# Kernel optimization log

Hardware: AMD Instinct MI355X
Metric: run time of the kernel (lower is better)

## Reference

```python
import jax, jax.numpy as jnp
import numpy as np

N_NODES = 50000
N_EDGES = 800000
N_GRAPHS = 128


def _gcn_conv(x, W, b, src, dst, n_nodes):
    # PyG GCNConv: h = x @ W; add self-loops; symmetric norm; aggregate; + bias
    h = x @ W  # [N, out]
    loop = jnp.arange(n_nodes, dtype=src.dtype)
    src_all = jnp.concatenate([src, loop])  # source (row)
    dst_all = jnp.concatenate([dst, loop])  # target (col)
    ones = jnp.ones(src_all.shape[0], dtype=h.dtype)
    deg = jax.ops.segment_sum(ones, dst_all, num_segments=n_nodes)  # in-degree w/ self loops
    dis = jnp.where(deg > 0, jax.lax.rsqrt(deg), 0.0)
    norm = dis[src_all] * dis[dst_all]  # [E+N]
    msg = norm[:, None] * h[src_all]  # [E+N, out]
    out = jax.ops.segment_sum(msg, dst_all, num_segments=n_nodes)
    return out + b


def setup_inputs() -> dict:
    key = jax.random.key(0)
    ks = jax.random.split(key, 7)
    x = jax.random.normal(ks[0], (N_NODES, 4), dtype=jnp.float32)
    edge_index = jax.random.randint(ks[1], (2, N_EDGES), 0, N_NODES, dtype=jnp.int64)
    batch = jnp.sort(jax.random.randint(ks[2], (N_NODES,), 0, N_GRAPHS, dtype=jnp.int64))
    # Glorot-ish init for the linear weights, zeros for bias (PyG default)
    W1 = jax.random.normal(ks[3], (4, 64), dtype=jnp.float32) * (1.0 / np.sqrt(4))
    b1 = jnp.zeros((64,), dtype=jnp.float32)
    W2 = jax.random.normal(ks[4], (64, 64), dtype=jnp.float32) * (1.0 / np.sqrt(64))
    b2 = jnp.zeros((64,), dtype=jnp.float32)
    return {"x": x, "edge_index": edge_index, "batch": batch, "num_graphs": N_GRAPHS,
            "W1": W1, "b1": b1, "W2": W2, "b2": b2}


def reference(x, edge_index, batch, num_graphs, W1, b1, W2, b2):
    src, dst = edge_index[0], edge_index[1]
    n = x.shape[0]
    h = jax.nn.relu(_gcn_conv(x, W1, b1, src, dst, n))
    h = jax.nn.relu(_gcn_conv(h, W2, b2, src, dst, n))
    # global_mean_pool: segment mean over graph ids
    sums = jax.ops.segment_sum(h, batch, num_segments=num_graphs)  # [G, 64]
    cnts = jax.ops.segment_sum(jnp.ones((n,), dtype=h.dtype), batch, num_segments=num_graphs)
    return sums / jnp.maximum(cnts, 1.0)[:, None]
```

## Files before the change

### kernel.cpp

```cpp
#include <hip/hip_runtime.h>
#include <hip/hip_fp16.h>

#define NG 128
#define CHUNK 4096

__device__ __forceinline__ int wave_iscan(int v, int lane) {
#pragma unroll
  for (int off = 1; off < 64; off <<= 1) {
    int u = __shfl_up(v, off, 64);
    if (lane >= off) v += u;
  }
  return v;
}


__global__ void bsum_kernel(const int* __restrict__ src, int* __restrict__ bsum, int M) {
  __shared__ int wsum[4];
  int tid = threadIdx.x, lane = tid & 63, wid = tid >> 6;
  int i = blockIdx.x * 256 + tid;
  int v = (i < M) ? src[i] : 0;
  int inc = wave_iscan(v, lane);
  if (lane == 63) wsum[wid] = inc;
  __syncthreads();
  if (tid == 0) bsum[blockIdx.x] = wsum[0] + wsum[1] + wsum[2] + wsum[3];
}

__global__ void bscan_kernel(int* __restrict__ bsum, int nb) {
  __shared__ int wsum[16];
  int tid = threadIdx.x, lane = tid & 63, wid = tid >> 6;
  int v = (tid < nb) ? bsum[tid] : 0;
  int inc = wave_iscan(v, lane);
  if (lane == 63) wsum[wid] = inc;
  __syncthreads();
  if (tid == 0) {
    int a = 0;
#pragma unroll
    for (int w = 0; w < 16; ++w) { int t = wsum[w]; wsum[w] = a; a += t; }
  }
  __syncthreads();
  if (tid < nb) bsum[tid] = inc - v + wsum[wid];
}

__global__ void offadd_kernel(int* __restrict__ off, const int* __restrict__ bsum, int M) {
  __shared__ int wsum[4];
  int tid = threadIdx.x, lane = tid & 63, wid = tid >> 6;
  int i = blockIdx.x * 256 + tid;
  int v = (i < M) ? off[i] : 0;
  int inc = wave_iscan(v, lane);
  if (lane == 63) wsum[wid] = inc;
  __syncthreads();
  if (tid == 0) {
    int a = bsum[blockIdx.x];
#pragma unroll
    for (int w = 0; w < 4; ++w) { int t = wsum[w]; wsum[w] = a; a += t; }
  }
  __syncthreads();
  if (i < M) off[i] = inc - v + wsum[wid];
}


__global__ void hist_kernel(const int* __restrict__ ei, int E, int nblkE, int K,
                            int* __restrict__ off) {
  __shared__ int lh[256];
  int tid = threadIdx.x, blk = blockIdx.x;
  lh[tid] = 0;
  __syncthreads();
  int e0 = blk * CHUNK;
  const int4* d4 = (const int4*)(ei + E + e0);
  for (int i = tid; i < CHUNK / 4; i += 256) {
    int base = e0 + 4 * i;
    if (base + 3 < E) {
      int4 d = d4[i];
      atomicAdd(&lh[d.x >> 8], 1);
      atomicAdd(&lh[d.y >> 8], 1);
      atomicAdd(&lh[d.z >> 8], 1);
      atomicAdd(&lh[d.w >> 8], 1);
    } else {
#pragma unroll
      for (int j = 0; j < 4; ++j) {
        int e = base + j;
        if (e < E) atomicAdd(&lh[ei[E + e] >> 8], 1);
      }
    }
  }
  __syncthreads();
  if (tid < K) off[tid * nblkE + blk] = lh[tid];
}

__global__ void part_kernel(const int* __restrict__ ei, int E, int nblkE, int K,
                            const int* __restrict__ off, unsigned int* __restrict__ epack) {
  __shared__ int lcur[256];
  int tid = threadIdx.x, blk = blockIdx.x;
  if (tid < K) lcur[tid] = off[tid * nblkE + blk];
  __syncthreads();
  int e0 = blk * CHUNK;
  const int4* s4 = (const int4*)(ei + e0);
  const int4* d4 = (const int4*)(ei + E + e0);
  for (int i = tid; i < CHUNK / 4; i += 256) {
    int base = e0 + 4 * i;
    if (base + 3 < E) {
      int4 s = s4[i];
      int4 d = d4[i];
#pragma unroll
      for (int j = 0; j < 4; ++j) {
        unsigned int ss = (unsigned int)((j == 0) ? s.x : (j == 1) ? s.y : (j == 2) ? s.z : s.w);
        unsigned int dd = (unsigned int)((j == 0) ? d.x : (j == 1) ? d.y : (j == 2) ? d.z : d.w);
        int pos = atomicAdd(&lcur[dd >> 8], 1);
        epack[pos] = (ss << 8) | (dd & 255u);
      }
    } else {
#pragma unroll
      for (int j = 0; j < 4; ++j) {
        int e = base + j;
        if (e < E) {
          unsigned int ss = (unsigned int)ei[e], dd = (unsigned int)ei[E + e];
          int pos = atomicAdd(&lcur[dd >> 8], 1);
          epack[pos] = (ss << 8) | (dd & 255u);
        }
      }
    }
  }
}

__global__ void csr2_kernel(const int* __restrict__ off, int nblkE, int K,
                            const unsigned int* __restrict__ epack,
                            const float* __restrict__ x, int* __restrict__ deg,
                            int* __restrict__ rowptr, float* __restrict__ dis,
                            float* __restrict__ xs, unsigned short* __restrict__ esrc,
                            int N, int E) {
  __shared__ int lcnt[256];
  __shared__ int lcur[256];
  __shared__ int wsum[4];
  int tid = threadIdx.x, b = blockIdx.x;
  int lane = tid & 63, wid = tid >> 6;
  lcnt[tid] = 0;
  __syncthreads();
  int be0 = off[b * nblkE];
  int be1 = (b + 1 < K) ? off[(b + 1) * nblkE] : E;
  for (int i = be0 + tid; i < be1; i += 256) atomicAdd(&lcnt[epack[i] & 255u], 1);
  __syncthreads();
  int v = lcnt[tid];
  int inc = wave_iscan(v, lane);
  if (lane == 63) wsum[wid] = inc;
  __syncthreads();
  if (tid == 0) {
    int a = be0;
#pragma unroll
    for (int w = 0; w < 4; ++w) { int t = wsum[w]; wsum[w] = a; a += t; }
  }
  __syncthreads();
  int exc = inc - v + wsum[wid];
  lcur[tid] = exc;
  int node = (b << 8) + tid;
  if (node < N) {
    rowptr[node] = exc;
    deg[node] = v;
    float di = rsqrtf((float)v + 1.0f);
    dis[node] = di;
    float4 xv = ((const float4*)x)[node];
    ((float4*)xs)[node] = make_float4(di * xv.x, di * xv.y, di * xv.z, di * xv.w);
  }
  __syncthreads();
  for (int i = be0 + tid; i < be1; i += 256) {
    unsigned int pk = epack[i];
    int pos = atomicAdd(&lcur[pk & 255u], 1);
    esrc[pos] = (unsigned short)(pk >> 8);
  }
}

__global__ void __launch_bounds__(256, 8)
l1_kernel(const int* __restrict__ rowptr, const int* __restrict__ deg,
          const unsigned short* __restrict__ esrc, const float* __restrict__ xs,
          const float* __restrict__ x, const float* __restrict__ dis,
          const float* __restrict__ W1, const float* __restrict__ b1,
          __half* __restrict__ h1p, int N) {
  int tid = threadIdx.x;
  int lane = tid & 63, wid = tid >> 6;
  int d = __builtin_amdgcn_readfirstlane(blockIdx.x * 4 + wid);
  if (d >= N) return;
  float di = dis[d];
  int p = __builtin_amdgcn_readfirstlane(rowptr[d]);
  int n = __builtin_amdgcn_readfirstlane(deg[d]);
  float a0 = 0.f, a1 = 0.f, a2 = 0.f, a3 = 0.f;
  for (int k = lane; k < n; k += 64) {
    int e = esrc[p + k];
    float4 v = ((const float4*)xs)[e];
    a0 += v.x; a1 += v.y; a2 += v.z; a3 += v.w;
  }
  if (lane == 0) {
    float4 xv = ((const float4*)x)[d];
    a0 = fmaf(di, xv.x, a0); a1 = fmaf(di, xv.y, a1);
    a2 = fmaf(di, xv.z, a2); a3 = fmaf(di, xv.w, a3);
  }
#pragma unroll
  for (int off = 1; off < 64; off <<= 1) {
    a0 += __shfl_xor(a0, off, 64);
    a1 += __shfl_xor(a1, off, 64);
    a2 += __shfl_xor(a2, off, 64);
    a3 += __shfl_xor(a3, off, 64);
  }
  a0 *= di; a1 *= di; a2 *= di; a3 *= di;
  float o = b1[lane] + a0 * W1[lane] + a1 * W1[64 + lane] + a2 * W1[128 + lane] + a3 * W1[192 + lane];
  h1p[(size_t)d * 64 + lane] = __float2half(di * fmaxf(o, 0.0f));
}

__global__ void __launch_bounds__(256, 8)
l2_kernel(const int* __restrict__ rowptr, const int* __restrict__ deg,
          const unsigned short* __restrict__ esrc, const __half* __restrict__ h1p,
          const float* __restrict__ dis, const float* __restrict__ W2,
          const float* __restrict__ b2, const int* __restrict__ batch,
          float* __restrict__ gsum, int N) {
  __shared__ __align__(16) unsigned short ebuf[4][64];
  __shared__ float vbuf[4][64];
  __shared__ float obuf[4][64];
  __shared__ int gbuf[4];
  int tid = threadIdx.x;
  int lane = tid & 63, wid = tid >> 6;
  int g = lane >> 3, c = lane & 7;
  int d0 = blockIdx.x * 4 + wid;
  bool valid = d0 < N;
  int d = __builtin_amdgcn_readfirstlane(valid ? d0 : N - 1);
  float di = dis[d];
  int p = __builtin_amdgcn_readfirstlane(rowptr[d]);
  int n = __builtin_amdgcn_readfirstlane(deg[d]);
  float a0, a1, a2, a3, a4, a5, a6, a7;
  {
    float ms = (g == 0) ? 1.0f : 0.0f;
    uint4 w = *(const uint4*)(h1p + (size_t)d * 64 + 8 * c);
    float2 f0 = __half22float2(*(__half2*)&w.x);
    float2 f1 = __half22float2(*(__half2*)&w.y);
    float2 f2 = __half22float2(*(__half2*)&w.z);
    float2 f3 = __half22float2(*(__half2*)&w.w);
    a0 = ms * f0.x; a1 = ms * f0.y; a2 = ms * f1.x; a3 = ms * f1.y;
    a4 = ms * f2.x; a5 = ms * f2.y; a6 = ms * f3.x; a7 = ms * f3.y;
  }
  for (int base = 0; base < n; base += 64) {
    int m64 = n - base;
    if (m64 > 64) m64 = 64;
    ebuf[wid][lane] = esrc[p + base + ((lane < m64) ? lane : (m64 - 1))];
    for (int k = 0; k < m64; k += 8) {
      int e = ebuf[wid][k + g];
      float m = (k + g < m64) ? 1.0f : 0.0f;
      uint4 w = *(const uint4*)(h1p + (size_t)e * 64 + 8 * c);
      float2 f0 = __half22float2(*(__half2*)&w.x);
      float2 f1 = __half22float2(*(__half2*)&w.y);
      float2 f2 = __half22float2(*(__half2*)&w.z);
      float2 f3 = __half22float2(*(__half2*)&w.w);
      a0 = fmaf(m, f0.x, a0); a1 = fmaf(m, f0.y, a1);
      a2 = fmaf(m, f1.x, a2); a3 = fmaf(m, f1.y, a3);
      a4 = fmaf(m, f2.x, a4); a5 = fmaf(m, f2.y, a5);
      a6 = fmaf(m, f3.x, a6); a7 = fmaf(m, f3.y, a7);
    }
  }
#pragma unroll
  for (int off = 8; off < 64; off <<= 1) {
    a0 += __shfl_xor(a0, off, 64); a1 += __shfl_xor(a1, off, 64);
    a2 += __shfl_xor(a2, off, 64); a3 += __shfl_xor(a3, off, 64);
    a4 += __shfl_xor(a4, off, 64); a5 += __shfl_xor(a5, off, 64);
    a6 += __shfl_xor(a6, off, 64); a7 += __shfl_xor(a7, off, 64);
  }
  if (g == 0) {
    *(float4*)&vbuf[wid][8 * c] = make_float4(di * a0, di * a1, di * a2, di * a3);
    *(float4*)&vbuf[wid][8 * c + 4] = make_float4(di * a4, di * a5, di * a6, di * a7);
  }
  float o = b2[lane];
  const float4* vb4 = (const float4*)vbuf[wid];
#pragma unroll
  for (int kk = 0; kk < 16; ++kk) {
    float4 vv = vb4[kk];
    o = fmaf(vv.x, W2[(kk * 4 + 0) * 64 + lane], o);
    o = fmaf(vv.y, W2[(kk * 4 + 1) * 64 + lane], o);
    o = fmaf(vv.z, W2[(kk * 4 + 2) * 64 + lane], o);
    o = fmaf(vv.w, W2[(kk * 4 + 3) * 64 + lane], o);
  }
  obuf[wid][lane] = fmaxf(o, 0.0f);
  if (lane == 0) gbuf[wid] = valid ? batch[d] : -1;
  __syncthreads();
  if (wid == 0) {
    float s = 0.0f;
    int cur = gbuf[0];
#pragma unroll
    for (int r = 0; r < 4; ++r) {
      int gg = gbuf[r];
      if (gg != cur) {
        if (cur >= 0) atomicAdd(&gsum[cur * 64 + lane], s);
        s = 0.0f;
        cur = gg;
      }
      if (gg >= 0) s += obuf[r][lane];
    }
    if (cur >= 0) atomicAdd(&gsum[cur * 64 + lane], s);
  }
}


__device__ __forceinline__ int lbound(const int* __restrict__ a, int n, int v) {
  int lo = 0, hi = n;
  while (lo < hi) {
    int mid = (lo + hi) >> 1;
    if (a[mid] < v) lo = mid + 1; else hi = mid;
  }
  return lo;
}

__global__ void out_kernel(const float* __restrict__ gsum, const int* __restrict__ batch,
                           int N, float* __restrict__ out) {
  int t = blockIdx.x * blockDim.x + threadIdx.x;
  if (t >= NG * 64) return;
  int g = t >> 6;
  int cnt = lbound(batch, N, g + 1) - lbound(batch, N, g);
  out[t] = gsum[t] / fmaxf((float)cnt, 1.0f);
}


extern "C" void kernel_launch(void* const* d_in, const int* in_sizes, int n_in,
                              void* d_out, int out_size, void* d_ws, size_t ws_size,
                              hipStream_t stream) {
  const float* x = (const float*)d_in[0];
  const int* ei = (const int*)d_in[1];
  const int* batch = (const int*)d_in[2];
  const float* W1 = (const float*)d_in[4];
  const float* b1 = (const float*)d_in[5];
  const float* W2 = (const float*)d_in[6];
  const float* b2 = (const float*)d_in[7];

  const int N = in_sizes[0] / 4;
  const int E = in_sizes[1] / 2;
  const int K = (N + 255) >> 8;
  const int nblkE = (E + CHUNK - 1) / CHUNK;
  const int M2 = K * nblkE;
  const int NB2 = (M2 + 255) / 256;

  float* gsum = (float*)d_ws;
  int* deg = (int*)(gsum + 64 * NG);
  int* rowptr = deg + N;
  float* xs = (float*)(rowptr + N);
  float* dis = xs + (size_t)4 * N;
  __half* h1p = (__half*)(dis + N);
  unsigned short* esrc = (unsigned short*)(dis + N + (size_t)32 * N);
  int* off = (int*)(esrc + E);
  int* bsum2 = off + M2;
  unsigned int* epack = (unsigned int*)(bsum2 + 1024);

  hipMemsetAsync(d_ws, 0, (size_t)64 * NG * 4, stream);

  const int B = 256;
  hist_kernel<<<nblkE, 256, 0, stream>>>(ei, E, nblkE, K, off);
  bsum_kernel<<<NB2, 256, 0, stream>>>(off, bsum2, M2);
  bscan_kernel<<<1, 1024, 0, stream>>>(bsum2, NB2);
  offadd_kernel<<<NB2, 256, 0, stream>>>(off, bsum2, M2);
  part_kernel<<<nblkE, 256, 0, stream>>>(ei, E, nblkE, K, off, epack);
  csr2_kernel<<<K, 256, 0, stream>>>(off, nblkE, K, epack, x, deg, rowptr, dis, xs, esrc, N, E);
  l1_kernel<<<(N + 3) / 4, 256, 0, stream>>>(rowptr, deg, esrc, xs, x, dis, W1, b1, h1p, N);
  l2_kernel<<<(N + 3) / 4, 256, 0, stream>>>(rowptr, deg, esrc, h1p, dis, W2, b2, batch, gsum, N);
  out_kernel<<<(NG * 64 + B - 1) / B, B, 0, stream>>>(gsum, batch, N, (float*)d_out);
}
```

Baseline: 104.4 us.

## Replace three-kernel offset scan with global bucket counts and atomic cursors

The per-chunk-per-bucket offset matrix and its three-kernel multi-block scan are replaced by global bucket counts accumulated with atomics, a single small scan kernel, and a partition kernel that recomputes its local histogram and reserves ranges through atomics on global bucket cursors. This removes two kernel launches and the large offset array traffic. In exchange the partition kernel reads destination indices twice, and edge order within a bucket now depends on atomic ordering, so the result is no longer deterministic.

```diff
diff --git a/kernel.cpp b/kernel.cpp
--- a/kernel.cpp
+++ b/kernel.cpp
@@ -13,54 +13,8 @@
   return v;
 }
 
-
-__global__ void bsum_kernel(const int* __restrict__ src, int* __restrict__ bsum, int M) {
-  __shared__ int wsum[4];
-  int tid = threadIdx.x, lane = tid & 63, wid = tid >> 6;
-  int i = blockIdx.x * 256 + tid;
-  int v = (i < M) ? src[i] : 0;
-  int inc = wave_iscan(v, lane);
-  if (lane == 63) wsum[wid] = inc;
-  __syncthreads();
-  if (tid == 0) bsum[blockIdx.x] = wsum[0] + wsum[1] + wsum[2] + wsum[3];
-}
-
-__global__ void bscan_kernel(int* __restrict__ bsum, int nb) {
-  __shared__ int wsum[16];
-  int tid = threadIdx.x, lane = tid & 63, wid = tid >> 6;
-  int v = (tid < nb) ? bsum[tid] : 0;
-  int inc = wave_iscan(v, lane);
-  if (lane == 63) wsum[wid] = inc;
-  __syncthreads();
-  if (tid == 0) {
-    int a = 0;
-#pragma unroll
-    for (int w = 0; w < 16; ++w) { int t = wsum[w]; wsum[w] = a; a += t; }
-  }
-  __syncthreads();
-  if (tid < nb) bsum[tid] = inc - v + wsum[wid];
-}
-
-__global__ void offadd_kernel(int* __restrict__ off, const int* __restrict__ bsum, int M) {
-  __shared__ int wsum[4];
-  int tid = threadIdx.x, lane = tid & 63, wid = tid >> 6;
-  int i = blockIdx.x * 256 + tid;
-  int v = (i < M) ? off[i] : 0;
-  int inc = wave_iscan(v, lane);
-  if (lane == 63) wsum[wid] = inc;
-  __syncthreads();
-  if (tid == 0) {
-    int a = bsum[blockIdx.x];
-#pragma unroll
-    for (int w = 0; w < 4; ++w) { int t = wsum[w]; wsum[w] = a; a += t; }
-  }
-  __syncthreads();
-  if (i < M) off[i] = inc - v + wsum[wid];
-}
-
-
-__global__ void hist_kernel(const int* __restrict__ ei, int E, int nblkE, int K,
-                            int* __restrict__ off) {
+__global__ void hist2_kernel(const int* __restrict__ ei, int E, int K,
+                             int* __restrict__ gcnt) {
   __shared__ int lh[256];
   int tid = threadIdx.x, blk = blockIdx.x;
   lh[tid] = 0;
@@ -84,14 +38,39 @@
     }
   }
   __syncthreads();
-  if (tid < K) off[tid * nblkE + blk] = lh[tid];
-}
-
-__global__ void part_kernel(const int* __restrict__ ei, int E, int nblkE, int K,
-                            const int* __restrict__ off, unsigned int* __restrict__ epack) {
-  __shared__ int lcur[256];
+  if (tid < K) {
+    int c = lh[tid];
+    if (c) atomicAdd(&gcnt[tid], c);
+  }
+}
+
+__global__ void scanK_kernel(const int* __restrict__ gcnt, int* __restrict__ bbase,
+                             int* __restrict__ bcur, int K) {
+  __shared__ int wsum[4];
+  int tid = threadIdx.x;
+  int lane = tid & 63, wid = tid >> 6;
+  int v = (tid < K) ? gcnt[tid] : 0;
+  int inc = wave_iscan(v, lane);
+  if (lane == 63) wsum[wid] = inc;
+  __syncthreads();
+  if (tid == 0) {
+    int a = 0;
+#pragma unroll
+    for (int w = 0; w < 4; ++w) { int t = wsum[w]; wsum[w] = a; a += t; }
+  }
+  __syncthreads();
+  if (tid < K) {
+    int exc = inc - v + wsum[wid];
+    bbase[tid] = exc;
+    bcur[tid] = exc;
+  }
+}
+
+__global__ void part_kernel(const int* __restrict__ ei, int E, int K,
+                            int* __restrict__ bcur, unsigned int* __restrict__ epack) {
+  __shared__ int lh[256];
   int tid = threadIdx.x, blk = blockIdx.x;
-  if (tid < K) lcur[tid] = off[tid * nblkE + blk];
+  lh[tid] = 0;
   __syncthreads();
   int e0 = blk * CHUNK;
   const int4* s4 = (const int4*)(ei + e0);
@@ -99,13 +78,35 @@
   for (int i = tid; i < CHUNK / 4; i += 256) {
     int base = e0 + 4 * i;
     if (base + 3 < E) {
+      int4 d = d4[i];
+      atomicAdd(&lh[d.x >> 8], 1);
+      atomicAdd(&lh[d.y >> 8], 1);
+      atomicAdd(&lh[d.z >> 8], 1);
+      atomicAdd(&lh[d.w >> 8], 1);
+    } else {
+#pragma unroll
+      for (int j = 0; j < 4; ++j) {
+        int e = base + j;
+        if (e < E) atomicAdd(&lh[ei[E + e] >> 8], 1);
+      }
+    }
+  }
+  __syncthreads();
+  if (tid < K) {
+    int c = lh[tid];
+    lh[tid] = c ? atomicAdd(&bcur[tid], c) : 0;
+  }
+  __syncthreads();
+  for (int i = tid; i < CHUNK / 4; i += 256) {
+    int base = e0 + 4 * i;
+    if (base + 3 < E) {
       int4 s = s4[i];
       int4 d = d4[i];
 #pragma unroll
       for (int j = 0; j < 4; ++j) {
         unsigned int ss = (unsigned int)((j == 0) ? s.x : (j == 1) ? s.y : (j == 2) ? s.z : s.w);
         unsigned int dd = (unsigned int)((j == 0) ? d.x : (j == 1) ? d.y : (j == 2) ? d.z : d.w);
-        int pos = atomicAdd(&lcur[dd >> 8], 1);
+        int pos = atomicAdd(&lh[dd >> 8], 1);
         epack[pos] = (ss << 8) | (dd & 255u);
       }
     } else {
@@ -114,7 +115,7 @@
         int e = base + j;
         if (e < E) {
           unsigned int ss = (unsigned int)ei[e], dd = (unsigned int)ei[E + e];
-          int pos = atomicAdd(&lcur[dd >> 8], 1);
+          int pos = atomicAdd(&lh[dd >> 8], 1);
           epack[pos] = (ss << 8) | (dd & 255u);
         }
       }
@@ -122,12 +123,12 @@
   }
 }
 
-__global__ void csr2_kernel(const int* __restrict__ off, int nblkE, int K,
+__global__ void csr2_kernel(const int* __restrict__ bbase, const int* __restrict__ gcnt,
                             const unsigned int* __restrict__ epack,
                             const float* __restrict__ x, int* __restrict__ deg,
                             int* __restrict__ rowptr, float* __restrict__ dis,
                             float* __restrict__ xs, unsigned short* __restrict__ esrc,
-                            int N, int E) {
+                            int N) {
   __shared__ int lcnt[256];
   __shared__ int lcur[256];
   __shared__ int wsum[4];
@@ -135,8 +136,8 @@
   int lane = tid & 63, wid = tid >> 6;
   lcnt[tid] = 0;
   __syncthreads();
-  int be0 = off[b * nblkE];
-  int be1 = (b + 1 < K) ? off[(b + 1) * nblkE] : E;
+  int be0 = bbase[b];
+  int be1 = be0 + gcnt[b];
   for (int i = be0 + tid; i < be1; i += 256) atomicAdd(&lcnt[epack[i] & 255u], 1);
   __syncthreads();
   int v = lcnt[tid];
@@ -328,29 +329,26 @@
   const int E = in_sizes[1] / 2;
   const int K = (N + 255) >> 8;
   const int nblkE = (E + CHUNK - 1) / CHUNK;
-  const int M2 = K * nblkE;
-  const int NB2 = (M2 + 255) / 256;
 
   float* gsum = (float*)d_ws;
-  int* deg = (int*)(gsum + 64 * NG);
+  int* gcnt = (int*)(gsum + 64 * NG);
+  int* bbase = gcnt + 256;
+  int* bcur = bbase + 256;
+  int* deg = bcur + 256;
   int* rowptr = deg + N;
   float* xs = (float*)(rowptr + N);
   float* dis = xs + (size_t)4 * N;
   __half* h1p = (__half*)(dis + N);
   unsigned short* esrc = (unsigned short*)(dis + N + (size_t)32 * N);
-  int* off = (int*)(esrc + E);
-  int* bsum2 = off + M2;
-  unsigned int* epack = (unsigned int*)(bsum2 + 1024);
-
-  hipMemsetAsync(d_ws, 0, (size_t)64 * NG * 4, stream);
+  unsigned int* epack = (unsigned int*)(esrc + E);
+
+  hipMemsetAsync(d_ws, 0, (size_t)(64 * NG + 256) * 4, stream);
 
   const int B = 256;
-  hist_kernel<<<nblkE, 256, 0, stream>>>(ei, E, nblkE, K, off);
-  bsum_kernel<<<NB2, 256, 0, stream>>>(off, bsum2, M2);
-  bscan_kernel<<<1, 1024, 0, stream>>>(bsum2, NB2);
-  offadd_kernel<<<NB2, 256, 0, stream>>>(off, bsum2, M2);
-  part_kernel<<<nblkE, 256, 0, stream>>>(ei, E, nblkE, K, off, epack);
-  csr2_kernel<<<K, 256, 0, stream>>>(off, nblkE, K, epack, x, deg, rowptr, dis, xs, esrc, N, E);
+  hist2_kernel<<<nblkE, 256, 0, stream>>>(ei, E, K, gcnt);
+  scanK_kernel<<<1, 256, 0, stream>>>(gcnt, bbase, bcur, K);
+  part_kernel<<<nblkE, 256, 0, stream>>>(ei, E, K, bcur, epack);
+  csr2_kernel<<<K, 256, 0, stream>>>(bbase, gcnt, epack, x, deg, rowptr, dis, xs, esrc, N);
   l1_kernel<<<(N + 3) / 4, 256, 0, stream>>>(rowptr, deg, esrc, xs, x, dis, W1, b1, h1p, N);
   l2_kernel<<<(N + 3) / 4, 256, 0, stream>>>(rowptr, deg, esrc, h1p, dis, W2, b2, batch, gsum, N);
   out_kernel<<<(NG * 64 + B - 1) / B, B, 0, stream>>>(gsum, batch, N, (float*)d_out);
```

Result: slower. 106.6 us (+2.1%).

## Fuse CSR build stages into one cooperative kernel with grid syncs

Applied to the files above, without the earlier changes.

Merges the histogram, three-pass offset scan, partition and per-bucket CSR kernels into one cooperative kernel separated by grid-wide barriers. The scan is restructured into a per-row reduction, a single-block scan of row sums, and a per-row local scan, which drops the separate block-sum buffer. This removes five kernel launches and the gaps between them. In exchange it adds five grid.sync barriers and relies on cooperative launch residency. The scan assumes nblkE and K are at most 256.

```diff
diff --git a/kernel.cpp b/kernel.cpp
--- a/kernel.cpp
+++ b/kernel.cpp
@@ -1,5 +1,8 @@
 #include <hip/hip_runtime.h>
 #include <hip/hip_fp16.h>
+#include <hip/hip_cooperative_groups.h>
+
+namespace cg = cooperative_groups;
 
 #define NG 128
 #define CHUNK 4096
@@ -13,158 +16,154 @@
   return v;
 }
 
-
-__global__ void bsum_kernel(const int* __restrict__ src, int* __restrict__ bsum, int M) {
+__global__ void coop_csr_kernel(const int* __restrict__ ei, int E, int K, int nblkE,
+                                int* __restrict__ off, int* __restrict__ rowsum,
+                                int* __restrict__ bbase, const float* __restrict__ x,
+                                int* __restrict__ deg, int* __restrict__ rowptr,
+                                float* __restrict__ dis, float* __restrict__ xs,
+                                unsigned short* __restrict__ esrc,
+                                unsigned int* __restrict__ epack, int N) {
+  cg::grid_group grid = cg::this_grid();
+  __shared__ int lh[256];
+  __shared__ int lcur[256];
   __shared__ int wsum[4];
-  int tid = threadIdx.x, lane = tid & 63, wid = tid >> 6;
-  int i = blockIdx.x * 256 + tid;
-  int v = (i < M) ? src[i] : 0;
-  int inc = wave_iscan(v, lane);
-  if (lane == 63) wsum[wid] = inc;
-  __syncthreads();
-  if (tid == 0) bsum[blockIdx.x] = wsum[0] + wsum[1] + wsum[2] + wsum[3];
-}
-
-__global__ void bscan_kernel(int* __restrict__ bsum, int nb) {
-  __shared__ int wsum[16];
-  int tid = threadIdx.x, lane = tid & 63, wid = tid >> 6;
-  int v = (tid < nb) ? bsum[tid] : 0;
-  int inc = wave_iscan(v, lane);
-  if (lane == 63) wsum[wid] = inc;
-  __syncthreads();
-  if (tid == 0) {
-    int a = 0;
-#pragma unroll
-    for (int w = 0; w < 16; ++w) { int t = wsum[w]; wsum[w] = a; a += t; }
-  }
-  __syncthreads();
-  if (tid < nb) bsum[tid] = inc - v + wsum[wid];
-}
-
-__global__ void offadd_kernel(int* __restrict__ off, const int* __restrict__ bsum, int M) {
-  __shared__ int wsum[4];
-  int tid = threadIdx.x, lane = tid & 63, wid = tid >> 6;
-  int i = blockIdx.x * 256 + tid;
-  int v = (i < M) ? off[i] : 0;
-  int inc = wave_iscan(v, lane);
-  if (lane == 63) wsum[wid] = inc;
-  __syncthreads();
-  if (tid == 0) {
-    int a = bsum[blockIdx.x];
-#pragma unroll
-    for (int w = 0; w < 4; ++w) { int t = wsum[w]; wsum[w] = a; a += t; }
-  }
-  __syncthreads();
-  if (i < M) off[i] = inc - v + wsum[wid];
-}
-
-
-__global__ void hist_kernel(const int* __restrict__ ei, int E, int nblkE, int K,
-                            int* __restrict__ off) {
-  __shared__ int lh[256];
-  int tid = threadIdx.x, blk = blockIdx.x;
-  lh[tid] = 0;
-  __syncthreads();
-  int e0 = blk * CHUNK;
-  const int4* d4 = (const int4*)(ei + E + e0);
-  for (int i = tid; i < CHUNK / 4; i += 256) {
-    int base = e0 + 4 * i;
-    if (base + 3 < E) {
-      int4 d = d4[i];
-      atomicAdd(&lh[d.x >> 8], 1);
-      atomicAdd(&lh[d.y >> 8], 1);
-      atomicAdd(&lh[d.z >> 8], 1);
-      atomicAdd(&lh[d.w >> 8], 1);
-    } else {
-#pragma unroll
-      for (int j = 0; j < 4; ++j) {
-        int e = base + j;
-        if (e < E) atomicAdd(&lh[ei[E + e] >> 8], 1);
+  int tid = threadIdx.x, bid = blockIdx.x;
+  int lane = tid & 63, wid = tid >> 6;
+
+  if (bid < nblkE) {
+    lh[tid] = 0;
+    __syncthreads();
+    int e0 = bid * CHUNK;
+    const int4* d4 = (const int4*)(ei + E + e0);
+    for (int i = tid; i < CHUNK / 4; i += 256) {
+      int base = e0 + 4 * i;
+      if (base + 3 < E) {
+        int4 d = d4[i];
+        atomicAdd(&lh[d.x >> 8], 1);
+        atomicAdd(&lh[d.y >> 8], 1);
+        atomicAdd(&lh[d.z >> 8], 1);
+        atomicAdd(&lh[d.w >> 8], 1);
+      } else {
+#pragma unroll
+        for (int j = 0; j < 4; ++j) {
+          int e = base + j;
+          if (e < E) atomicAdd(&lh[ei[E + e] >> 8], 1);
+        }
       }
     }
-  }
-  __syncthreads();
-  if (tid < K) off[tid * nblkE + blk] = lh[tid];
-}
-
-__global__ void part_kernel(const int* __restrict__ ei, int E, int nblkE, int K,
-                            const int* __restrict__ off, unsigned int* __restrict__ epack) {
-  __shared__ int lcur[256];
-  int tid = threadIdx.x, blk = blockIdx.x;
-  if (tid < K) lcur[tid] = off[tid * nblkE + blk];
-  __syncthreads();
-  int e0 = blk * CHUNK;
-  const int4* s4 = (const int4*)(ei + e0);
-  const int4* d4 = (const int4*)(ei + E + e0);
-  for (int i = tid; i < CHUNK / 4; i += 256) {
-    int base = e0 + 4 * i;
-    if (base + 3 < E) {
-      int4 s = s4[i];
-      int4 d = d4[i];
-#pragma unroll
-      for (int j = 0; j < 4; ++j) {
-        unsigned int ss = (unsigned int)((j == 0) ? s.x : (j == 1) ? s.y : (j == 2) ? s.z : s.w);
-        unsigned int dd = (unsigned int)((j == 0) ? d.x : (j == 1) ? d.y : (j == 2) ? d.z : d.w);
-        int pos = atomicAdd(&lcur[dd >> 8], 1);
-        epack[pos] = (ss << 8) | (dd & 255u);
-      }
-    } else {
-#pragma unroll
-      for (int j = 0; j < 4; ++j) {
-        int e = base + j;
-        if (e < E) {
-          unsigned int ss = (unsigned int)ei[e], dd = (unsigned int)ei[E + e];
+    __syncthreads();
+    if (tid < K) off[tid * nblkE + bid] = lh[tid];
+  }
+  grid.sync();
+
+  if (bid < K) {
+    int v = (tid < nblkE) ? off[bid * nblkE + tid] : 0;
+#pragma unroll
+    for (int o = 1; o < 64; o <<= 1) v += __shfl_xor(v, o, 64);
+    if (lane == 0) wsum[wid] = v;
+    __syncthreads();
+    if (tid == 0) rowsum[bid] = wsum[0] + wsum[1] + wsum[2] + wsum[3];
+  }
+  grid.sync();
+
+  if (bid == 0) {
+    int v = (tid < K) ? rowsum[tid] : 0;
+    int inc = wave_iscan(v, lane);
+    if (lane == 63) wsum[wid] = inc;
+    __syncthreads();
+    if (tid == 0) {
+      int a = 0;
+#pragma unroll
+      for (int w = 0; w < 4; ++w) { int t = wsum[w]; wsum[w] = a; a += t; }
+      bbase[K] = E;
+    }
+    __syncthreads();
+    if (tid < K) bbase[tid] = inc - v + wsum[wid];
+  }
+  grid.sync();
+
+  if (bid < K) {
+    int v = (tid < nblkE) ? off[bid * nblkE + tid] : 0;
+    int inc = wave_iscan(v, lane);
+    if (lane == 63) wsum[wid] = inc;
+    __syncthreads();
+    if (tid == 0) {
+      int a = bbase[bid];
+#pragma unroll
+      for (int w = 0; w < 4; ++w) { int t = wsum[w]; wsum[w] = a; a += t; }
+    }
+    __syncthreads();
+    if (tid < nblkE) off[bid * nblkE + tid] = inc - v + wsum[wid];
+  }
+  grid.sync();
+
+  if (bid < nblkE) {
+    if (tid < K) lcur[tid] = off[tid * nblkE + bid];
+    __syncthreads();
+    int e0 = bid * CHUNK;
+    const int4* s4 = (const int4*)(ei + e0);
+    const int4* d4 = (const int4*)(ei + E + e0);
+    for (int i = tid; i < CHUNK / 4; i += 256) {
+      int base = e0 + 4 * i;
+      if (base + 3 < E) {
+        int4 s = s4[i];
+        int4 d = d4[i];
+#pragma unroll
+        for (int j = 0; j < 4; ++j) {
+          unsigned int ss = (unsigned int)((j == 0) ? s.x : (j == 1) ? s.y : (j == 2) ? s.z : s.w);
+          unsigned int dd = (unsigned int)((j == 0) ? d.x : (j == 1) ? d.y : (j == 2) ? d.z : d.w);
           int pos = atomicAdd(&lcur[dd >> 8], 1);
           epack[pos] = (ss << 8) | (dd & 255u);
         }
+      } else {
+#pragma unroll
+        for (int j = 0; j < 4; ++j) {
+          int e = base + j;
+          if (e < E) {
+            unsigned int ss = (unsigned int)ei[e], dd = (unsigned int)ei[E + e];
+            int pos = atomicAdd(&lcur[dd >> 8], 1);
+            epack[pos] = (ss << 8) | (dd & 255u);
+          }
+        }
       }
     }
   }
-}
-
-__global__ void csr2_kernel(const int* __restrict__ off, int nblkE, int K,
-                            const unsigned int* __restrict__ epack,
-                            const float* __restrict__ x, int* __restrict__ deg,
-                            int* __restrict__ rowptr, float* __restrict__ dis,
-                            float* __restrict__ xs, unsigned short* __restrict__ esrc,
-                            int N, int E) {
-  __shared__ int lcnt[256];
-  __shared__ int lcur[256];
-  __shared__ int wsum[4];
-  int tid = threadIdx.x, b = blockIdx.x;
-  int lane = tid & 63, wid = tid >> 6;
-  lcnt[tid] = 0;
-  __syncthreads();
-  int be0 = off[b * nblkE];
-  int be1 = (b + 1 < K) ? off[(b + 1) * nblkE] : E;
-  for (int i = be0 + tid; i < be1; i += 256) atomicAdd(&lcnt[epack[i] & 255u], 1);
-  __syncthreads();
-  int v = lcnt[tid];
-  int inc = wave_iscan(v, lane);
-  if (lane == 63) wsum[wid] = inc;
-  __syncthreads();
-  if (tid == 0) {
-    int a = be0;
-#pragma unroll
-    for (int w = 0; w < 4; ++w) { int t = wsum[w]; wsum[w] = a; a += t; }
-  }
-  __syncthreads();
-  int exc = inc - v + wsum[wid];
-  lcur[tid] = exc;
-  int node = (b << 8) + tid;
-  if (node < N) {
-    rowptr[node] = exc;
-    deg[node] = v;
-    float di = rsqrtf((float)v + 1.0f);
-    dis[node] = di;
-    float4 xv = ((const float4*)x)[node];
-    ((float4*)xs)[node] = make_float4(di * xv.x, di * xv.y, di * xv.z, di * xv.w);
-  }
-  __syncthreads();
-  for (int i = be0 + tid; i < be1; i += 256) {
-    unsigned int pk = epack[i];
-    int pos = atomicAdd(&lcur[pk & 255u], 1);
-    esrc[pos] = (unsigned short)(pk >> 8);
+  grid.sync();
+
+  if (bid < K) {
+    lh[tid] = 0;
+    __syncthreads();
+    int be0 = bbase[bid];
+    int be1 = bbase[bid + 1];
+    for (int i = be0 + tid; i < be1; i += 256) atomicAdd(&lh[epack[i] & 255u], 1);
+    __syncthreads();
+    int v = lh[tid];
+    int inc = wave_iscan(v, lane);
+    if (lane == 63) wsum[wid] = inc;
+    __syncthreads();
+    if (tid == 0) {
+      int a = be0;
+#pragma unroll
+      for (int w = 0; w < 4; ++w) { int t = wsum[w]; wsum[w] = a; a += t; }
+    }
+    __syncthreads();
+    int exc = inc - v + wsum[wid];
+    lcur[tid] = exc;
+    int node = (bid << 8) + tid;
+    if (node < N) {
+      rowptr[node] = exc;
+      deg[node] = v;
+      float di = rsqrtf((float)v + 1.0f);
+      dis[node] = di;
+      float4 xv = ((const float4*)x)[node];
+      ((float4*)xs)[node] = make_float4(di * xv.x, di * xv.y, di * xv.z, di * xv.w);
+    }
+    __syncthreads();
+    for (int i = be0 + tid; i < be1; i += 256) {
+      unsigned int pk = epack[i];
+      int pos = atomicAdd(&lcur[pk & 255u], 1);
+      esrc[pos] = (unsigned short)(pk >> 8);
+    }
   }
 }
 
@@ -328,29 +327,35 @@
   const int E = in_sizes[1] / 2;
   const int K = (N + 255) >> 8;
   const int nblkE = (E + CHUNK - 1) / CHUNK;
+  const int GRID = (K > nblkE) ? K : nblkE;
   const int M2 = K * nblkE;
-  const int NB2 = (M2 + 255) / 256;
 
   float* gsum = (float*)d_ws;
-  int* deg = (int*)(gsum + 64 * NG);
+  int* rowsum = (int*)(gsum + 64 * NG);
+  int* bbase = rowsum + 256;
+  int* deg = bbase + 260;
   int* rowptr = deg + N;
   float* xs = (float*)(rowptr + N);
   float* dis = xs + (size_t)4 * N;
   __half* h1p = (__half*)(dis + N);
   unsigned short* esrc = (unsigned short*)(dis + N + (size_t)32 * N);
   int* off = (int*)(esrc + E);
-  int* bsum2 = off + M2;
-  unsigned int* epack = (unsigned int*)(bsum2 + 1024);
+  unsigned int* epack = (unsigned int*)(off + M2);
 
   hipMemsetAsync(d_ws, 0, (size_t)64 * NG * 4, stream);
 
   const int B = 256;
-  hist_kernel<<<nblkE, 256, 0, stream>>>(ei, E, nblkE, K, off);
-  bsum_kernel<<<NB2, 256, 0, stream>>>(off, bsum2, M2);
-  bscan_kernel<<<1, 1024, 0, stream>>>(bsum2, NB2);
-  offadd_kernel<<<NB2, 256, 0, stream>>>(off, bsum2, M2);
-  part_kernel<<<nblkE, 256, 0, stream>>>(ei, E, nblkE, K, off, epack);
-  csr2_kernel<<<K, 256, 0, stream>>>(off, nblkE, K, epack, x, deg, rowptr, dis, xs, esrc, N, E);
+  {
+    int E_ = E, K_ = K, nblkE_ = nblkE, N_ = N;
+    const int* ei_ = ei;
+    const float* x_ = x;
+    void* args[] = {(void*)&ei_, (void*)&E_, (void*)&K_, (void*)&nblkE_,
+                    (void*)&off, (void*)&rowsum, (void*)&bbase, (void*)&x_,
+                    (void*)&deg, (void*)&rowptr, (void*)&dis, (void*)&xs,
+                    (void*)&esrc, (void*)&epack, (void*)&N_};
+    hipLaunchCooperativeKernel((const void*)coop_csr_kernel, dim3(GRID), dim3(256),
+                               args, 0, stream);
+  }
   l1_kernel<<<(N + 3) / 4, 256, 0, stream>>>(rowptr, deg, esrc, xs, x, dis, W1, b1, h1p, N);
   l2_kernel<<<(N + 3) / 4, 256, 0, stream>>>(rowptr, deg, esrc, h1p, dis, W2, b2, batch, gsum, N);
   out_kernel<<<(NG * 64 + B - 1) / B, B, 0, stream>>>(gsum, batch, N, (float*)d_out);
```

New measurement: 225.0 us. 2.15x slower.
